# Kernel tuning notes

Measured on AMD Instinct MI355X. Metric: run time of the kernel, lower is better.

The kernel has to match this reference:

```python
import jax, jax.numpy as jnp
import numpy as np
from jax.ops import segment_sum, segment_max

DIM = 64; EDGE_DIM = 6; ACTION_DIM = 6
N = 16384; E = 32768; G = 256; TPG = 12  # nodes, edges, graphs, torsions/graph


def setup_inputs() -> dict:
    key = jax.random.key(0)
    ks = jax.random.split(key, 16)
    d = DIM
    def lin(k, fo, fi):
        return (jax.random.normal(k, (fo, fi), jnp.float32) / np.sqrt(fi)).astype(jnp.float32)
    return {
        "x": jax.random.normal(ks[0], (N, 3), jnp.float32),
        "edge_attr": jax.random.normal(ks[1], (E, EDGE_DIM), jnp.float32),
        "edge_index": jax.random.randint(ks[2], (2, E), 0, N),
        "batch": (jnp.arange(N) // (N // G)).astype(jnp.int32),
        "nonring": jax.random.randint(ks[3], (G * TPG, 4), 0, N),
        "nrbidx": (jnp.arange(G * TPG) // TPG).astype(jnp.int32),
        "num_graphs": G,
        "torsion_size": TPG,
        "lin0_w": lin(ks[4], d, 3), "lin0_b": jnp.zeros((d,), jnp.float32),
        "e1_w": lin(ks[5], d, EDGE_DIM), "e1_b": jnp.zeros((d,), jnp.float32),
        "e2_w": lin(ks[6], d * d, d), "e2_b": jnp.zeros((d * d,), jnp.float32),
        "root_w": lin(ks[7], d, d), "conv_b": jnp.zeros((d,), jnp.float32),
        "gru_wih": lin(ks[8], 3 * d, d), "gru_whh": lin(ks[9], 3 * d, d),
        "gru_bih": jnp.zeros((3 * d,), jnp.float32), "gru_bhh": jnp.zeros((3 * d,), jnp.float32),
        "s2s_wih": lin(ks[10], 4 * d, 2 * d), "s2s_whh": lin(ks[11], 4 * d, d),
        "s2s_bih": jnp.zeros((4 * d,), jnp.float32), "s2s_bhh": jnp.zeros((4 * d,), jnp.float32),
        "mem_wih": lin(ks[12], 4 * d, 2 * d), "mem_whh": lin(ks[13], 4 * d, d),
        "mem_bih": jnp.zeros((4 * d,), jnp.float32), "mem_bhh": jnp.zeros((4 * d,), jnp.float32),
        "lin1_w": lin(ks[14], d, 5 * d), "lin1_b": jnp.zeros((d,), jnp.float32),
        "lin2_w": lin(ks[15], ACTION_DIM, d), "lin2_b": jnp.zeros((ACTION_DIM,), jnp.float32),
    }


def _lstm_step(xin, h, c, wih, whh, bih, bhh):
    g = xin @ wih.T + bih + h @ whh.T + bhh
    i, f, gg, o = jnp.split(g, 4, axis=-1)
    c = jax.nn.sigmoid(f) * c + jax.nn.sigmoid(i) * jnp.tanh(gg)
    h = jax.nn.sigmoid(o) * jnp.tanh(c)
    return h, c


def _model(x, edge_attr, lin0_w, lin0_b, e1_w, e1_b, e2_w, e2_b, root_w, conv_b,
           gru_wih, gru_whh, gru_bih, gru_bhh, s2s_wih, s2s_whh, s2s_bih, s2s_bhh,
           mem_wih, mem_whh, mem_bih, mem_bhh, lin1_w, lin1_b, lin2_w, lin2_b,
           edge_index, batch, nonring, nrbidx, num_graphs, torsion_size):
    d = lin0_w.shape[0]
    n = x.shape[0]
    out = jax.nn.relu(x @ lin0_w.T + lin0_b)           # [N, d]
    h = out                                            # GRU hidden
    src, dst = edge_index[0], edge_index[1]
    # edge-conditioned weights (fixed across the 6 iterations -> computed once)
    ew = (jax.nn.relu(edge_attr @ e1_w.T + e1_b) @ e2_w.T + e2_b).reshape(-1, d, d)  # [E, d, d]
    deg = jnp.clip(segment_sum(jnp.ones((src.shape[0],), out.dtype), dst, num_segments=n), 1.0)
    for _ in range(6):
        msg = jnp.einsum('ei,eio->eo', out[src], ew)   # per-edge matmul, [E, d]
        agg = segment_sum(msg, dst, num_segments=n) / deg[:, None]  # scatter-mean
        m = jax.nn.relu(agg + out @ root_w + conv_b)
        gi = m @ gru_wih.T + gru_bih
        gh = h @ gru_whh.T + gru_bhh
        r = jax.nn.sigmoid(gi[:, :d] + gh[:, :d])
        z = jax.nn.sigmoid(gi[:, d:2 * d] + gh[:, d:2 * d])
        nnew = jnp.tanh(gi[:, 2 * d:] + r * gh[:, 2 * d:])
        h = (1.0 - z) * nnew + z * h
        out = h
    # Set2Set pooling, 6 processing steps
    q_star = jnp.zeros((num_graphs, 2 * d), out.dtype)
    hs = jnp.zeros((num_graphs, d), out.dtype); cs = jnp.zeros_like(hs)
    for _ in range(6):
        hs, cs = _lstm_step(q_star, hs, cs, s2s_wih, s2s_whh, s2s_bih, s2s_bhh)
        e = jnp.sum(out * hs[batch], axis=-1)
        emax = segment_max(e, batch, num_segments=num_graphs)
        a = jnp.exp(e - emax[batch])
        a = a / segment_sum(a, batch, num_segments=num_graphs)[batch]
        r_ = segment_sum(a[:, None] * out, batch, num_segments=num_graphs)
        q_star = jnp.concatenate([hs, r_], axis=-1)
    # memory LSTM, single step from zero state
    hx = jnp.zeros((num_graphs, d), out.dtype); cx = jnp.zeros_like(hx)
    hx, cx = _lstm_step(q_star, hx, cx, mem_wih, mem_whh, mem_bih, mem_bhh)
    lstm_sel = hx[nrbidx]                                   # [T, d]
    node_sel = out[nonring.reshape(-1)].reshape(4, -1, d)   # faithful to .view(4,-1,dim)
    stacked = jnp.concatenate([lstm_sel[None], node_sel], axis=0)  # [5, T, d]
    feat = jnp.transpose(stacked, (2, 1, 0)).reshape(-1, 5 * d)    # faithful permute+reshape -> [T, 5d]
    o1 = jax.nn.relu(feat @ lin1_w.T + lin1_b)
    logits = o1 @ lin2_w.T + lin2_b                          # [T, action_dim]
    logit = logits.reshape(num_graphs, torsion_size, -1)     # uniform split + pad_sequence
    return logit, hx[None], cx[None]


def reference(x, edge_attr, edge_index, batch, nonring, nrbidx, num_graphs, torsion_size,
              lin0_w, lin0_b, e1_w, e1_b, e2_w, e2_b, root_w, conv_b,
              gru_wih, gru_whh, gru_bih, gru_bhh, s2s_wih, s2s_whh, s2s_bih, s2s_bhh,
              mem_wih, mem_whh, mem_bih, mem_bhh, lin1_w, lin1_b, lin2_w, lin2_b):
    return _model(x, edge_attr, lin0_w, lin0_b, e1_w, e1_b, e2_w, e2_b, root_w, conv_b,
                  gru_wih, gru_whh, gru_bih, gru_bhh, s2s_wih, s2s_whh, s2s_bih, s2s_bhh,
                  mem_wih, mem_whh, mem_bih, mem_bhh, lin1_w, lin1_b, lin2_w, lin2_b,
                  edge_index, batch, nonring, nrbidx, num_graphs, torsion_size)
```

## Files before the change

kernel.cpp:

```cpp
#include <hip/hip_runtime.h>

#define NNODE 16384
#define NEDGE 32768
#define NG    256
#define TPGx  12
#define TTOT  (NG * TPGx)
#define D     64

typedef _Float16 h8 __attribute__((ext_vector_type(8)));
typedef _Float16 h4 __attribute__((ext_vector_type(4)));
typedef float    f4 __attribute__((ext_vector_type(4)));

static __device__ __forceinline__ float sigm(float x) { return 1.f / (1.f + __expf(-x)); }

static __device__ __forceinline__ f4 mfma16h(h8 a, h8 b, f4 c) {
  return __builtin_amdgcn_mfma_f32_16x16x32_f16(a, b, c, 0, 0, 0);
}

static __device__ __forceinline__ h8 splat16(_Float16 x) {
  h8 v = {x, x, x, x, x, x, x, x};
  return v;
}

#define WS_H      0
#define WS_AGG    4194304
#define WS_W2     8388608
#define WS_RT     8921088
#define WS_WHH    8929280
#define WS_WIH    8953856
#define WS_SWIHT  8978432
#define WS_SWHHT  9109504
#define WS_MWIHT  9175040
#define WS_L1WT   9306112
#define WS_L2WF   9388032
#define WS_FB     9389568
#define WS_DEG    9398784
#define WS_HX     9464320
#define WS_NEED   9529856

struct Srcs { const void* p[23]; };

__device__ __constant__ const int kCum[24] = {
    0, 192, 256, 640, 704, 262848, 266944, 271040, 271104, 283392, 295680,
    295872, 296064, 328832, 345216, 345472, 345728, 378496, 378752, 379008,
    399488, 399552, 399936, 399942};

__global__ __launch_bounds__(256) void pack_kernel(Srcs S, char* __restrict__ ws) {
  int idx = blockIdx.x * 256 + threadIdx.x;
  if (idx >= 399942) return;
  int r = 0, base = 0;
#pragma unroll
  for (int k = 0; k < 23; k++)
    if (idx >= kCum[k]) { r = k; base = kCum[k]; }
  int li = idx - base;
  float v = ((const float*)S.p[r])[li];

  float*    fb    = (float*)(ws + WS_FB);
  _Float16* w2    = (_Float16*)(ws + WS_W2);
  _Float16* rtH   = (_Float16*)(ws + WS_RT);
  _Float16* whhH  = (_Float16*)(ws + WS_WHH);
  _Float16* wihH  = (_Float16*)(ws + WS_WIH);
  float*    swihT = (float*)(ws + WS_SWIHT);
  float*    swhhT = (float*)(ws + WS_SWHHT);
  float*    mwihT = (float*)(ws + WS_MWIHT);
  float*    l1wT  = (float*)(ws + WS_L1WT);
  float*    l2w   = (float*)(ws + WS_L2WF);

  switch (r) {
    case 0: fb[li] = v; break;
    case 1: fb[192 + li] = v; break;
    case 2: fb[256 + li] = v; break;
    case 3: fb[640 + li] = v; break;
    case 4: {
      int i = li >> 12, o = (li >> 6) & 63, k = li & 63;
      w2[i * 4096 + (((k >> 3) * 64 + o) << 3) + (k & 7)] = (_Float16)v;
    } break;
    case 5: {
      int k = li >> 6, o = li & 63;
      w2[64 * 4096 + (((k >> 3) * 64 + o) << 3) + (k & 7)] = (_Float16)v;
    } break;
    case 6: {
      int i = li >> 6, o = li & 63;
      rtH[o * 64 + i] = (_Float16)v;
    } break;
    case 7: fb[704 + li] = v; break;
    case 8: wihH[li] = (_Float16)v; break;
    case 9: whhH[li] = (_Float16)v; break;
    case 10: fb[768 + li] = v; break;
    case 11: fb[960 + li] = v; break;
    case 12: swihT[(li & 127) * 256 + (li >> 7)] = v; break;
    case 13: swhhT[(li & 63) * 256 + (li >> 6)] = v; break;
    case 14: fb[1152 + li] = v; break;
    case 15: fb[1408 + li] = v; break;
    case 16: mwihT[(li & 127) * 256 + (li >> 7)] = v; break;
    case 17: fb[1664 + li] = v; break;
    case 18: fb[1920 + li] = v; break;
    case 19: l1wT[(li % 320) * 64 + (li / 320)] = v; break;
    case 20: fb[2176 + li] = v; break;
    case 21: l2w[li] = v; break;
    case 22: fb[2240 + li] = v; break;
  }
}

__global__ __launch_bounds__(256) void init_kernel(
    const float* __restrict__ x, const float* __restrict__ fb,
    float* __restrict__ h) {
  int idx = blockIdx.x * 256 + threadIdx.x;
  int n = idx >> 6, o = idx & 63;
  float acc = fb[192 + o];
#pragma unroll
  for (int j = 0; j < 3; j++) acc += x[n * 3 + j] * fb[o * 3 + j];
  h[idx] = fmaxf(acc, 0.f);
}

__global__ __launch_bounds__(256) void deg_kernel(const int* __restrict__ edge_index,
                                                  float* __restrict__ deg) {
  int e = blockIdx.x * 256 + threadIdx.x;
  if (e < NEDGE) atomicAdd(&deg[edge_index[NEDGE + e]], 1.0f);
}

__global__ __launch_bounds__(256) void msg_kernel(
    const float* __restrict__ h, const float* __restrict__ ea,
    const float* __restrict__ fb, const _Float16* __restrict__ w2,
    const int* __restrict__ edge_index, float* __restrict__ agg) {
  __shared__ _Float16 sOut[64][72];
  const int tid = threadIdx.x;
  const int wave = tid >> 6, lane = tid & 63;
  const int m15 = lane & 15, quad = lane >> 4;
  const int eb = blockIdx.x * 64;
  {
    int r = tid >> 2, c0 = (tid & 3) * 16;
    int srcn = edge_index[eb + r];
#pragma unroll
    for (int c = c0; c < c0 + 16; c += 4) {
      float4 v = *(const float4*)&h[srcn * D + c];
      sOut[r][c]     = (_Float16)v.x;
      sOut[r][c + 1] = (_Float16)v.y;
      sOut[r][c + 2] = (_Float16)v.z;
      sOut[r][c + 3] = (_Float16)v.w;
    }
  }
  h8 hid0[4], hid1[4];
#pragma unroll
  for (int r = 0; r < 4; r++) {
    int e = eb + r * 16 + m15;
    float eav[6];
#pragma unroll
    for (int j = 0; j < 6; j++) eav[j] = ea[e * 6 + j];
#pragma unroll
    for (int j = 0; j < 8; j++) {
      int k0 = quad * 8 + j, k1 = 32 + quad * 8 + j;
      float a0 = fb[640 + k0], a1 = fb[640 + k1];
#pragma unroll
      for (int jj = 0; jj < 6; jj++) {
        a0 += eav[jj] * fb[256 + k0 * 6 + jj];
        a1 += eav[jj] * fb[256 + k1 * 6 + jj];
      }
      hid0[r][j] = (_Float16)fmaxf(a0, 0.f);
      hid1[r][j] = (_Float16)fmaxf(a1, 0.f);
    }
  }
  __syncthreads();
  const _Float16* bp0 = w2 + (quad * 64 + wave * 16 + m15) * 8;
  const _Float16* bp1 = w2 + ((4 + quad) * 64 + wave * 16 + m15) * 8;
  f4 zz = {0.f, 0.f, 0.f, 0.f};
  f4 acc[4];
#pragma unroll
  for (int r = 0; r < 4; r++) acc[r] = zz;
  h8 c0[4], c1[4];
#pragma unroll
  for (int t = 0; t < 4; t++) {
    c0[t] = *(const h8*)(bp0 + t * 4096);
    c1[t] = *(const h8*)(bp1 + t * 4096);
  }
#pragma unroll
  for (int p = 0; p < 16; p++) {
    h8 n0[4], n1[4];
    if (p < 15) {
#pragma unroll
      for (int t = 0; t < 4; t++) {
        int i = (p + 1) * 4 + t;
        n0[t] = *(const h8*)(bp0 + i * 4096);
        n1[t] = *(const h8*)(bp1 + i * 4096);
      }
    }
#pragma unroll
    for (int r = 0; r < 4; r++) {
      h4 os4 = *(const h4*)&sOut[r * 16 + m15][p * 4];
#pragma unroll
      for (int t = 0; t < 4; t++) {
        h8 os = splat16(os4[t]);
        acc[r] = mfma16h(hid0[r] * os, c0[t], acc[r]);
        acc[r] = mfma16h(hid1[r] * os, c1[t], acc[r]);
      }
    }
    if (p < 15) {
#pragma unroll
      for (int t = 0; t < 4; t++) { c0[t] = n0[t]; c1[t] = n1[t]; }
    }
  }
  {
    h8 b0 = *(const h8*)(bp0 + 64 * 4096);
    h8 b1 = *(const h8*)(bp1 + 64 * 4096);
#pragma unroll
    for (int r = 0; r < 4; r++) {
      h8 a0 = *(const h8*)&sOut[r * 16 + m15][quad * 8];
      h8 a1 = *(const h8*)&sOut[r * 16 + m15][32 + quad * 8];
      acc[r] = mfma16h(a0, b0, acc[r]);
      acc[r] = mfma16h(a1, b1, acc[r]);
    }
  }
#pragma unroll
  for (int r = 0; r < 4; r++) {
#pragma unroll
    for (int reg = 0; reg < 4; reg++) {
      int ee = eb + r * 16 + quad * 4 + reg;
      int dn = edge_index[NEDGE + ee];
      atomicAdd(agg + dn * D + wave * 16 + m15, acc[r][reg]);
    }
  }
}

__global__ __launch_bounds__(256) void update_kernel(
    float* __restrict__ h, float* __restrict__ agg, const float* __restrict__ deg,
    const _Float16* __restrict__ rtH, const _Float16* __restrict__ whhH,
    const _Float16* __restrict__ wihH, const float* __restrict__ fb) {
  __shared__ float buf[64][68];
  const int tid = threadIdx.x;
  const int wave = tid >> 6, lane = tid & 63;
  const int m15 = lane & 15, quad = lane >> 4;
  const int nb = blockIdx.x * 64;
  {
    int r = tid >> 2, c0 = (tid & 3) * 16;
#pragma unroll
    for (int c = c0; c < c0 + 16; c += 4)
      *(float4*)&buf[r][c] = *(const float4*)&h[(nb + r) * D + c];
  }
  __syncthreads();
  const int mrow = wave * 16 + m15;
  h8 a0, a1;
#pragma unroll
  for (int j = 0; j < 8; j++) {
    a0[j] = (_Float16)buf[mrow][quad * 8 + j];
    a1[j] = (_Float16)buf[mrow][32 + quad * 8 + j];
  }
  f4 zz = {0.f, 0.f, 0.f, 0.f};
  f4 acc[16];
#pragma unroll
  for (int nt = 0; nt < 16; nt++) acc[nt] = zz;
#pragma unroll
  for (int nt = 0; nt < 16; nt++) {
    int nn = nt * 16 + m15;
    const _Float16* bp = (nt < 4) ? (rtH + nn * D) : (whhH + (nn - 64) * D);
    h8 bh0 = *(const h8*)(bp + quad * 8);
    h8 bh1 = *(const h8*)(bp + 32 + quad * 8);
    f4 a = acc[nt];
    a = mfma16h(a0, bh0, a);
    a = mfma16h(a1, bh1, a);
    acc[nt] = a;
  }
  __syncthreads();
#pragma unroll
  for (int nt = 0; nt < 4; nt++) {
#pragma unroll
    for (int reg = 0; reg < 4; reg++) {
      int nloc = wave * 16 + quad * 4 + reg;
      int o = nt * 16 + m15;
      float dg = fmaxf(deg[nb + nloc], 1.f);
      int aidx = (nb + nloc) * D + o;
      float v = acc[nt][reg] + agg[aidx] / dg + fb[704 + o];
      agg[aidx] = 0.f;
      buf[nloc][o] = fmaxf(v, 0.f);
    }
  }
  __syncthreads();
  h8 m0, m1;
#pragma unroll
  for (int j = 0; j < 8; j++) {
    m0[j] = (_Float16)buf[mrow][quad * 8 + j];
    m1[j] = (_Float16)buf[mrow][32 + quad * 8 + j];
  }
  f4 g2[12];
#pragma unroll
  for (int nt = 0; nt < 12; nt++) g2[nt] = zz;
#pragma unroll
  for (int nt = 0; nt < 12; nt++) {
    int nn = nt * 16 + m15;
    const _Float16* bp = wihH + nn * D;
    h8 bh0 = *(const h8*)(bp + quad * 8);
    h8 bh1 = *(const h8*)(bp + 32 + quad * 8);
    f4 a = g2[nt];
    a = mfma16h(m0, bh0, a);
    a = mfma16h(m1, bh1, a);
    g2[nt] = a;
  }
#pragma unroll
  for (int nt = 0; nt < 4; nt++) {
#pragma unroll
    for (int reg = 0; reg < 4; reg++) {
      int nloc = wave * 16 + quad * 4 + reg;
      int o = nt * 16 + m15;
      int gidx = (nb + nloc) * D + o;
      float gir = g2[nt][reg]      + fb[768 + o];
      float giz = g2[nt + 4][reg]  + fb[768 + 64 + o];
      float gin = g2[nt + 8][reg]  + fb[768 + 128 + o];
      float ghr = acc[nt + 4][reg]  + fb[960 + o];
      float ghz = acc[nt + 8][reg]  + fb[960 + 64 + o];
      float ghn = acc[nt + 12][reg] + fb[960 + 128 + o];
      float rr = sigm(gir + ghr);
      float zg = sigm(giz + ghz);
      float nnv = tanhf(gin + rr * ghn);
      float hv = h[gidx];
      h[gidx] = (1.f - zg) * nnv + zg * hv;
    }
  }
}

__global__ __launch_bounds__(256) void s2s_kernel(
    const float* __restrict__ h,
    const float* __restrict__ wihT, const float* __restrict__ whhT,
    const float* __restrict__ mwihT, const float* __restrict__ fb,
    float* __restrict__ hx_f32, float* __restrict__ dout) {
  __shared__ float outL[64][65];
  __shared__ float qs[128];
  __shared__ float hsv[64], csv[64], sg[256], sa[64];
  __shared__ float spart[4][64];
  const int t = threadIdx.x;
  const int g = blockIdx.x;
  float wr[128];
#pragma unroll
  for (int j = 0; j < 128; j++) wr[j] = wihT[j * 256 + t];
  for (int idx = t; idx < 64 * 64; idx += 256) outL[idx >> 6][idx & 63] = h[g * 4096 + idx];
  if (t < 128) qs[t] = 0.f;
  if (t < 64) { hsv[t] = 0.f; csv[t] = 0.f; }
  __syncthreads();
  for (int step = 0; step < 6; step++) {
    float acc = fb[1152 + t] + fb[1408 + t];
#pragma unroll
    for (int j = 0; j < 128; j++) acc += qs[j] * wr[j];
#pragma unroll 8
    for (int j = 0; j < 64; j++) acc += hsv[j] * whhT[j * 256 + t];
    sg[t] = acc;
    __syncthreads();
    if (t < 64) {
      float cn = sigm(sg[64 + t]) * csv[t] + sigm(sg[t]) * tanhf(sg[128 + t]);
      csv[t] = cn;
      hsv[t] = sigm(sg[192 + t]) * tanhf(cn);
    }
    __syncthreads();
    if (t < 64) {
      float e = 0.f;
      for (int d2 = 0; d2 < 64; d2++) e += outL[t][d2] * hsv[d2];
      float mx = e;
      for (int off = 32; off > 0; off >>= 1) mx = fmaxf(mx, __shfl_xor(mx, off));
      float a = __expf(e - mx);
      float s = a;
      for (int off = 32; off > 0; off >>= 1) s += __shfl_xor(s, off);
      sa[t] = a / s;
    }
    __syncthreads();
    {
      int o = t & 63, part = t >> 6;
      float r = 0.f;
      for (int n2 = part * 16; n2 < part * 16 + 16; n2++) r += sa[n2] * outL[n2][o];
      spart[part][o] = r;
    }
    __syncthreads();
    if (t < 64) {
      qs[t] = hsv[t];
      qs[64 + t] = spart[0][t] + spart[1][t] + spart[2][t] + spart[3][t];
    }
    __syncthreads();
  }
  float acc = fb[1664 + t] + fb[1920 + t];
#pragma unroll 8
  for (int j = 0; j < 128; j++) acc += qs[j] * mwihT[j * 256 + t];
  sg[t] = acc;
  __syncthreads();
  if (t < 64) {
    float cn = sigm(sg[t]) * tanhf(sg[128 + t]);
    float hn = sigm(sg[192 + t]) * tanhf(cn);
    hx_f32[g * 64 + t] = hn;
    dout[TTOT * 6 + g * 64 + t] = hn;
    dout[TTOT * 6 + NG * 64 + g * 64 + t] = cn;
  }
}

__global__ __launch_bounds__(64) void head_kernel(
    const float* __restrict__ h, const float* __restrict__ hx_f32,
    const int* __restrict__ nonring, const int* __restrict__ nrbidx,
    const float* __restrict__ l1wT, const float* __restrict__ l2w,
    const float* __restrict__ fb, float* __restrict__ dout) {
  __shared__ float feat[320];
  __shared__ float so1[64];
  const int r = blockIdx.x;
  const int lane = threadIdx.x;
  const int blk = r % 48, di = r / 48;
  const int tt = blk * 64 + lane;
  feat[lane * 5] = hx_f32[nrbidx[tt] * 64 + di];
#pragma unroll
  for (int s = 1; s <= 4; s++)
    feat[lane * 5 + s] = h[nonring[(s - 1) * TTOT + tt] * 64 + di];
  __syncthreads();
  float acc = fb[2176 + lane];
#pragma unroll 8
  for (int c = 0; c < 320; c++) acc += feat[c] * l1wT[c * 64 + lane];
  so1[lane] = fmaxf(acc, 0.f);
  __syncthreads();
  if (lane < 6) {
    float a2 = fb[2240 + lane];
    for (int j = 0; j < 64; j++) a2 += so1[j] * l2w[lane * 64 + j];
    dout[r * 6 + lane] = a2;
  }
}

extern "C" void kernel_launch(void* const* d_in, const int* in_sizes, int n_in,
                              void* d_out, int out_size, void* d_ws, size_t ws_size,
                              hipStream_t stream) {
  (void)in_sizes; (void)n_in; (void)out_size;
  const float* x         = (const float*)d_in[0];
  const float* edge_attr = (const float*)d_in[1];
  const int* edge_index  = (const int*)d_in[2];
  const int* nonring     = (const int*)d_in[4];
  const int* nrbidx      = (const int*)d_in[5];
  float* out = (float*)d_out;

  char* ws = (char*)d_ws;
  float*    h      = (float*)(ws + WS_H);
  float*    agg    = (float*)(ws + WS_AGG);
  _Float16* w2     = (_Float16*)(ws + WS_W2);
  _Float16* rtH    = (_Float16*)(ws + WS_RT);
  _Float16* whhH   = (_Float16*)(ws + WS_WHH);
  _Float16* wihH   = (_Float16*)(ws + WS_WIH);
  float*    swihT  = (float*)(ws + WS_SWIHT);
  float*    swhhT  = (float*)(ws + WS_SWHHT);
  float*    mwihT  = (float*)(ws + WS_MWIHT);
  float*    l1wT   = (float*)(ws + WS_L1WT);
  float*    l2wF   = (float*)(ws + WS_L2WF);
  float*    fb     = (float*)(ws + WS_FB);
  float*    deg    = (float*)(ws + WS_DEG);
  float*    hx_f32 = (float*)(ws + WS_HX);
  if (ws_size < (size_t)WS_NEED) return;

  Srcs S;
  S.p[0] = d_in[8];   S.p[1] = d_in[9];   S.p[2] = d_in[10];  S.p[3] = d_in[11];
  S.p[4] = d_in[12];  S.p[5] = d_in[13];  S.p[6] = d_in[14];  S.p[7] = d_in[15];
  S.p[8] = d_in[16];  S.p[9] = d_in[17];  S.p[10] = d_in[18]; S.p[11] = d_in[19];
  S.p[12] = d_in[20]; S.p[13] = d_in[21]; S.p[14] = d_in[22]; S.p[15] = d_in[23];
  S.p[16] = d_in[24]; S.p[17] = d_in[26]; S.p[18] = d_in[27]; S.p[19] = d_in[28];
  S.p[20] = d_in[29]; S.p[21] = d_in[30]; S.p[22] = d_in[31];
  pack_kernel<<<(399942 + 255) / 256, 256, 0, stream>>>(S, ws);

  init_kernel<<<NNODE * D / 256, 256, 0, stream>>>(x, fb, h);
  hipMemsetAsync(deg, 0, NNODE * 4, stream);
  hipMemsetAsync(agg, 0, NNODE * D * 4, stream);
  deg_kernel<<<NEDGE / 256, 256, 0, stream>>>(edge_index, deg);

  for (int it = 0; it < 6; it++) {
    msg_kernel<<<NEDGE / 64, 256, 0, stream>>>(h, edge_attr, fb, w2, edge_index, agg);
    update_kernel<<<NNODE / 64, 256, 0, stream>>>(h, agg, deg, rtH, whhH, wihH, fb);
  }

  s2s_kernel<<<NG, 256, 0, stream>>>(h, swihT, swhhT, mwihT, fb, hx_f32, out);
  head_kernel<<<TTOT, 64, 0, stream>>>(h, hx_f32, nonring, nrbidx, l1wT, l2wF, fb, out);
}
```

Measured before the change: 443.4 us.

## Merge setup launches, shrink update blocks, fast tanh, fewer s2s barriers

Folds the pack, zero-fill, init and degree work into two setup kernels, replacing five launches plus two memsets. The update kernel now uses one-wave blocks of 16 nodes, so it needs fewer barriers and launches more blocks. tanhf is swapped for an exp-based tanh, and the s2s attention loop is collapsed so one 64-thread group does the readout serially, cutting barriers. Risks are tanh overflow for large inputs (exp going to inf yields NaN), the serial readout in s2s, and the update blocks reloading weights per 16 nodes.

```diff
diff --git a/kernel.cpp b/kernel.cpp
--- a/kernel.cpp
+++ b/kernel.cpp
@@ -12,6 +12,10 @@
 typedef float    f4 __attribute__((ext_vector_type(4)));
 
 static __device__ __forceinline__ float sigm(float x) { return 1.f / (1.f + __expf(-x)); }
+static __device__ __forceinline__ float tanh_f(float x) {
+  float t = __expf(2.f * x);
+  return (t - 1.f) / (t + 1.f);
+}
 
 static __device__ __forceinline__ f4 mfma16h(h8 a, h8 b, f4 c) {
   return __builtin_amdgcn_mfma_f32_16x16x32_f16(a, b, c, 0, 0, 0);
@@ -45,79 +49,97 @@
     295872, 296064, 328832, 345216, 345472, 345728, 378496, 378752, 379008,
     399488, 399552, 399936, 399942};
 
-__global__ __launch_bounds__(256) void pack_kernel(Srcs S, char* __restrict__ ws) {
+__global__ __launch_bounds__(256) void setup1_kernel(Srcs S, char* __restrict__ ws) {
   int idx = blockIdx.x * 256 + threadIdx.x;
-  if (idx >= 399942) return;
-  int r = 0, base = 0;
-#pragma unroll
-  for (int k = 0; k < 23; k++)
-    if (idx >= kCum[k]) { r = k; base = kCum[k]; }
-  int li = idx - base;
-  float v = ((const float*)S.p[r])[li];
-
-  float*    fb    = (float*)(ws + WS_FB);
-  _Float16* w2    = (_Float16*)(ws + WS_W2);
-  _Float16* rtH   = (_Float16*)(ws + WS_RT);
-  _Float16* whhH  = (_Float16*)(ws + WS_WHH);
-  _Float16* wihH  = (_Float16*)(ws + WS_WIH);
-  float*    swihT = (float*)(ws + WS_SWIHT);
-  float*    swhhT = (float*)(ws + WS_SWHHT);
-  float*    mwihT = (float*)(ws + WS_MWIHT);
-  float*    l1wT  = (float*)(ws + WS_L1WT);
-  float*    l2w   = (float*)(ws + WS_L2WF);
-
-  switch (r) {
-    case 0: fb[li] = v; break;
-    case 1: fb[192 + li] = v; break;
-    case 2: fb[256 + li] = v; break;
-    case 3: fb[640 + li] = v; break;
-    case 4: {
-      int i = li >> 12, o = (li >> 6) & 63, k = li & 63;
-      w2[i * 4096 + (((k >> 3) * 64 + o) << 3) + (k & 7)] = (_Float16)v;
-    } break;
-    case 5: {
-      int k = li >> 6, o = li & 63;
-      w2[64 * 4096 + (((k >> 3) * 64 + o) << 3) + (k & 7)] = (_Float16)v;
-    } break;
-    case 6: {
-      int i = li >> 6, o = li & 63;
-      rtH[o * 64 + i] = (_Float16)v;
-    } break;
-    case 7: fb[704 + li] = v; break;
-    case 8: wihH[li] = (_Float16)v; break;
-    case 9: whhH[li] = (_Float16)v; break;
-    case 10: fb[768 + li] = v; break;
-    case 11: fb[960 + li] = v; break;
-    case 12: swihT[(li & 127) * 256 + (li >> 7)] = v; break;
-    case 13: swhhT[(li & 63) * 256 + (li >> 6)] = v; break;
-    case 14: fb[1152 + li] = v; break;
-    case 15: fb[1408 + li] = v; break;
-    case 16: mwihT[(li & 127) * 256 + (li >> 7)] = v; break;
-    case 17: fb[1664 + li] = v; break;
-    case 18: fb[1920 + li] = v; break;
-    case 19: l1wT[(li % 320) * 64 + (li / 320)] = v; break;
-    case 20: fb[2176 + li] = v; break;
-    case 21: l2w[li] = v; break;
-    case 22: fb[2240 + li] = v; break;
-  }
-}
-
-__global__ __launch_bounds__(256) void init_kernel(
-    const float* __restrict__ x, const float* __restrict__ fb,
-    float* __restrict__ h) {
+  if (idx < 399942) {
+    int r = 0, base = 0;
+#pragma unroll
+    for (int k = 0; k < 23; k++)
+      if (idx >= kCum[k]) { r = k; base = kCum[k]; }
+    int li = idx - base;
+    float v = ((const float*)S.p[r])[li];
+
+    float*    fb    = (float*)(ws + WS_FB);
+    _Float16* w2    = (_Float16*)(ws + WS_W2);
+    _Float16* rtH   = (_Float16*)(ws + WS_RT);
+    _Float16* whhH  = (_Float16*)(ws + WS_WHH);
+    _Float16* wihH  = (_Float16*)(ws + WS_WIH);
+    float*    swihT = (float*)(ws + WS_SWIHT);
+    float*    swhhT = (float*)(ws + WS_SWHHT);
+    float*    mwihT = (float*)(ws + WS_MWIHT);
+    float*    l1wT  = (float*)(ws + WS_L1WT);
+    float*    l2w   = (float*)(ws + WS_L2WF);
+
+    switch (r) {
+      case 0: fb[li] = v; break;
+      case 1: fb[192 + li] = v; break;
+      case 2: fb[256 + li] = v; break;
+      case 3: fb[640 + li] = v; break;
+      case 4: {
+        int i = li >> 12, o = (li >> 6) & 63, k = li & 63;
+        w2[i * 4096 + (((k >> 3) * 64 + o) << 3) + (k & 7)] = (_Float16)v;
+      } break;
+      case 5: {
+        int k = li >> 6, o = li & 63;
+        w2[64 * 4096 + (((k >> 3) * 64 + o) << 3) + (k & 7)] = (_Float16)v;
+      } break;
+      case 6: {
+        int i = li >> 6, o = li & 63;
+        rtH[o * 64 + i] = (_Float16)v;
+      } break;
+      case 7: fb[704 + li] = v; break;
+      case 8: wihH[li] = (_Float16)v; break;
+      case 9: whhH[li] = (_Float16)v; break;
+      case 10: fb[768 + li] = v; break;
+      case 11: fb[960 + li] = v; break;
+      case 12: swihT[(li & 127) * 256 + (li >> 7)] = v; break;
+      case 13: swhhT[(li & 63) * 256 + (li >> 6)] = v; break;
+      case 14: fb[1152 + li] = v; break;
+      case 15: fb[1408 + li] = v; break;
+      case 16: mwihT[(li & 127) * 256 + (li >> 7)] = v; break;
+      case 17: fb[1664 + li] = v; break;
+      case 18: fb[1920 + li] = v; break;
+      case 19: l1wT[(li % 320) * 64 + (li / 320)] = v; break;
+      case 20: fb[2176 + li] = v; break;
+      case 21: l2w[li] = v; break;
+      case 22: fb[2240 + li] = v; break;
+    }
+    return;
+  }
+  idx -= 399942;
+  float4 z4 = {0.f, 0.f, 0.f, 0.f};
+  if (idx < 262144) { ((float4*)(ws + WS_AGG))[idx] = z4; return; }
+  idx -= 262144;
+  if (idx < 4096) ((float4*)(ws + WS_DEG))[idx] = z4;
+}
+#define SETUP1_N (399942 + 262144 + 4096)
+
+__global__ __launch_bounds__(256) void setup2_kernel(
+    const float* __restrict__ x, const int* __restrict__ edge_index,
+    char* __restrict__ ws) {
   int idx = blockIdx.x * 256 + threadIdx.x;
-  int n = idx >> 6, o = idx & 63;
-  float acc = fb[192 + o];
-#pragma unroll
-  for (int j = 0; j < 3; j++) acc += x[n * 3 + j] * fb[o * 3 + j];
-  h[idx] = fmaxf(acc, 0.f);
-}
-
-__global__ __launch_bounds__(256) void deg_kernel(const int* __restrict__ edge_index,
-                                                  float* __restrict__ deg) {
-  int e = blockIdx.x * 256 + threadIdx.x;
-  if (e < NEDGE) atomicAdd(&deg[edge_index[NEDGE + e]], 1.0f);
-}
+  if (idx < 262144) {
+    const float* fb = (const float*)(ws + WS_FB);
+    float* h = (float*)(ws + WS_H);
+    int n = idx >> 4, oq = idx & 15;
+    float x0 = x[n * 3], x1 = x[n * 3 + 1], x2 = x[n * 3 + 2];
+    float4 out;
+#pragma unroll
+    for (int c = 0; c < 4; c++) {
+      int o = oq * 4 + c;
+      float acc = fb[192 + o] + x0 * fb[o * 3] + x1 * fb[o * 3 + 1] + x2 * fb[o * 3 + 2];
+      ((float*)&out)[c] = fmaxf(acc, 0.f);
+    }
+    *(float4*)&h[n * 64 + oq * 4] = out;
+    return;
+  }
+  idx -= 262144;
+  if (idx < NEDGE) {
+    float* deg = (float*)(ws + WS_DEG);
+    atomicAdd(&deg[edge_index[NEDGE + idx]], 1.0f);
+  }
+}
+#define SETUP2_N (262144 + NEDGE)
 
 __global__ __launch_bounds__(256) void msg_kernel(
     const float* __restrict__ h, const float* __restrict__ ea,
@@ -221,28 +243,27 @@
   }
 }
 
-__global__ __launch_bounds__(256) void update_kernel(
+__global__ __launch_bounds__(64) void update_kernel(
     float* __restrict__ h, float* __restrict__ agg, const float* __restrict__ deg,
     const _Float16* __restrict__ rtH, const _Float16* __restrict__ whhH,
     const _Float16* __restrict__ wihH, const float* __restrict__ fb) {
-  __shared__ float buf[64][68];
-  const int tid = threadIdx.x;
-  const int wave = tid >> 6, lane = tid & 63;
+  __shared__ float bufH[16][68];
+  __shared__ float bufM[16][68];
+  const int lane = threadIdx.x;
   const int m15 = lane & 15, quad = lane >> 4;
-  const int nb = blockIdx.x * 64;
+  const int nb = blockIdx.x * 16;
   {
-    int r = tid >> 2, c0 = (tid & 3) * 16;
+    int r = lane >> 2, c0 = (lane & 3) * 16;
 #pragma unroll
     for (int c = c0; c < c0 + 16; c += 4)
-      *(float4*)&buf[r][c] = *(const float4*)&h[(nb + r) * D + c];
-  }
-  __syncthreads();
-  const int mrow = wave * 16 + m15;
+      *(float4*)&bufH[r][c] = *(const float4*)&h[(nb + r) * D + c];
+  }
+  __syncthreads();
   h8 a0, a1;
 #pragma unroll
   for (int j = 0; j < 8; j++) {
-    a0[j] = (_Float16)buf[mrow][quad * 8 + j];
-    a1[j] = (_Float16)buf[mrow][32 + quad * 8 + j];
+    a0[j] = (_Float16)bufH[m15][quad * 8 + j];
+    a1[j] = (_Float16)bufH[m15][32 + quad * 8 + j];
   }
   f4 zz = {0.f, 0.f, 0.f, 0.f};
   f4 acc[16];
@@ -259,26 +280,25 @@
     a = mfma16h(a1, bh1, a);
     acc[nt] = a;
   }
-  __syncthreads();
 #pragma unroll
   for (int nt = 0; nt < 4; nt++) {
 #pragma unroll
     for (int reg = 0; reg < 4; reg++) {
-      int nloc = wave * 16 + quad * 4 + reg;
+      int nloc = quad * 4 + reg;
       int o = nt * 16 + m15;
       float dg = fmaxf(deg[nb + nloc], 1.f);
       int aidx = (nb + nloc) * D + o;
       float v = acc[nt][reg] + agg[aidx] / dg + fb[704 + o];
       agg[aidx] = 0.f;
-      buf[nloc][o] = fmaxf(v, 0.f);
+      bufM[nloc][o] = fmaxf(v, 0.f);
     }
   }
   __syncthreads();
   h8 m0, m1;
 #pragma unroll
   for (int j = 0; j < 8; j++) {
-    m0[j] = (_Float16)buf[mrow][quad * 8 + j];
-    m1[j] = (_Float16)buf[mrow][32 + quad * 8 + j];
+    m0[j] = (_Float16)bufM[m15][quad * 8 + j];
+    m1[j] = (_Float16)bufM[m15][32 + quad * 8 + j];
   }
   f4 g2[12];
 #pragma unroll
@@ -298,7 +318,7 @@
   for (int nt = 0; nt < 4; nt++) {
 #pragma unroll
     for (int reg = 0; reg < 4; reg++) {
-      int nloc = wave * 16 + quad * 4 + reg;
+      int nloc = quad * 4 + reg;
       int o = nt * 16 + m15;
       int gidx = (nb + nloc) * D + o;
       float gir = g2[nt][reg]      + fb[768 + o];
@@ -309,7 +329,7 @@
       float ghn = acc[nt + 12][reg] + fb[960 + 128 + o];
       float rr = sigm(gir + ghr);
       float zg = sigm(giz + ghz);
-      float nnv = tanhf(gin + rr * ghn);
+      float nnv = tanh_f(gin + rr * ghn);
       float hv = h[gidx];
       h[gidx] = (1.f - zg) * nnv + zg * hv;
     }
@@ -324,7 +344,6 @@
   __shared__ float outL[64][65];
   __shared__ float qs[128];
   __shared__ float hsv[64], csv[64], sg[256], sa[64];
-  __shared__ float spart[4][64];
   const int t = threadIdx.x;
   const int g = blockIdx.x;
   float wr[128];
@@ -343,12 +362,10 @@
     sg[t] = acc;
     __syncthreads();
     if (t < 64) {
-      float cn = sigm(sg[64 + t]) * csv[t] + sigm(sg[t]) * tanhf(sg[128 + t]);
+      float cn = sigm(sg[64 + t]) * csv[t] + sigm(sg[t]) * tanh_f(sg[128 + t]);
       csv[t] = cn;
-      hsv[t] = sigm(sg[192 + t]) * tanhf(cn);
-    }
-    __syncthreads();
-    if (t < 64) {
+      float hv = sigm(sg[192 + t]) * tanh_f(cn);
+      hsv[t] = hv;
       float e = 0.f;
       for (int d2 = 0; d2 < 64; d2++) e += outL[t][d2] * hsv[d2];
       float mx = e;
@@ -357,18 +374,10 @@
       float s = a;
       for (int off = 32; off > 0; off >>= 1) s += __shfl_xor(s, off);
       sa[t] = a / s;
-    }
-    __syncthreads();
-    {
-      int o = t & 63, part = t >> 6;
       float r = 0.f;
-      for (int n2 = part * 16; n2 < part * 16 + 16; n2++) r += sa[n2] * outL[n2][o];
-      spart[part][o] = r;
-    }
-    __syncthreads();
-    if (t < 64) {
-      qs[t] = hsv[t];
-      qs[64 + t] = spart[0][t] + spart[1][t] + spart[2][t] + spart[3][t];
+      for (int n2 = 0; n2 < 64; n2++) r += sa[n2] * outL[n2][t];
+      qs[t] = hv;
+      qs[64 + t] = r;
     }
     __syncthreads();
   }
@@ -378,8 +387,8 @@
   sg[t] = acc;
   __syncthreads();
   if (t < 64) {
-    float cn = sigm(sg[t]) * tanhf(sg[128 + t]);
-    float hn = sigm(sg[192 + t]) * tanhf(cn);
+    float cn = sigm(sg[t]) * tanh_f(sg[128 + t]);
+    float hn = sigm(sg[192 + t]) * tanh_f(cn);
     hx_f32[g * 64 + t] = hn;
     dout[TTOT * 6 + g * 64 + t] = hn;
     dout[TTOT * 6 + NG * 64 + g * 64 + t] = cn;
@@ -449,16 +458,13 @@
   S.p[12] = d_in[20]; S.p[13] = d_in[21]; S.p[14] = d_in[22]; S.p[15] = d_in[23];
   S.p[16] = d_in[24]; S.p[17] = d_in[26]; S.p[18] = d_in[27]; S.p[19] = d_in[28];
   S.p[20] = d_in[29]; S.p[21] = d_in[30]; S.p[22] = d_in[31];
-  pack_kernel<<<(399942 + 255) / 256, 256, 0, stream>>>(S, ws);
-
-  init_kernel<<<NNODE * D / 256, 256, 0, stream>>>(x, fb, h);
-  hipMemsetAsync(deg, 0, NNODE * 4, stream);
-  hipMemsetAsync(agg, 0, NNODE * D * 4, stream);
-  deg_kernel<<<NEDGE / 256, 256, 0, stream>>>(edge_index, deg);
+
+  setup1_kernel<<<(SETUP1_N + 255) / 256, 256, 0, stream>>>(S, ws);
+  setup2_kernel<<<(SETUP2_N + 255) / 256, 256, 0, stream>>>(x, edge_index, ws);
 
   for (int it = 0; it < 6; it++) {
     msg_kernel<<<NEDGE / 64, 256, 0, stream>>>(h, edge_attr, fb, w2, edge_index, agg);
-    update_kernel<<<NNODE / 64, 256, 0, stream>>>(h, agg, deg, rtH, whhH, wihH, fb);
+    update_kernel<<<NNODE / 16, 64, 0, stream>>>(h, agg, deg, rtH, whhH, wihH, fb);
   }
 
   s2s_kernel<<<NG, 256, 0, stream>>>(h, swihT, swhhT, mwihT, fb, hx_f32, out);
```

Result: no change. 444.5 us (+0.2%).
